# Kernel optimization log

Hardware: AMD Instinct MI355X
Metric: run time of the kernel (lower is better)

## Reference

```python
import jax, jax.numpy as jnp
import numpy as np

B = 16384  # batch
D = 1024   # input_size (== hidden_size, required by the original code)
H = 1024   # hidden_size


def setup_inputs() -> dict:
    key = jax.random.key(0)
    ks = jax.random.split(key, 20)
    s = 0.02
    inp = {
        "x": jax.random.normal(ks[0], (B, D), dtype=jnp.float32),
        "h": jax.random.normal(ks[1], (B, H), dtype=jnp.float32),
        "c_prev": jax.random.normal(ks[2], (B, H), dtype=jnp.float32),
    }
    names = ["i_x", "f_x", "c_x", "o_x", "i_h", "f_h", "c_h", "o_h"]
    for n, name in enumerate(names):
        in_dim = D if name.endswith("_x") else H
        inp["W" + name] = jax.random.normal(ks[3 + 2 * n], (H, in_dim), dtype=jnp.float32) * s
        inp["b" + name] = jax.random.normal(ks[4 + 2 * n], (H,), dtype=jnp.float32) * s
    return inp


def reference(x, h, c_prev,
              Wi_x, bi_x, Wf_x, bf_x, Wc_x, bc_x, Wo_x, bo_x,
              Wi_h, bi_h, Wf_h, bf_h, Wc_h, bc_h, Wo_h, bo_h):
    # NOTE: the original module applies NO sigmoid to the gates; i, f, o are raw affine sums.
    i = x @ Wi_x.T + bi_x + h @ Wi_h.T + bi_h
    f = x @ Wf_x.T + bf_x + h @ Wf_h.T + bf_h
    g = jnp.tanh(x @ Wc_x.T + bc_x + h @ Wc_h.T + bc_h)
    o = x @ Wo_x.T + bo_x + h @ Wo_h.T + bo_h
    c_next = g * i + c_prev * f
    h_next = o * jnp.tanh(c_next)
    return (h_next, c_next)
```

## Files before the change

kernel.cpp:

```cpp
#include <hip/hip_runtime.h>
#include <hip/hip_bf16.h>


#define MROWS 16384
#define NCOLS 1024
#define KTOT  2048

typedef __attribute__((ext_vector_type(8))) short bf16x8;
typedef __attribute__((ext_vector_type(4))) float f32x4;
typedef unsigned int u32;
typedef unsigned short u16;

__device__ __forceinline__ u16 f2bf(float f) {
  union { float f; u32 u; } v; v.f = f;
  u32 r = v.u + 0x7fffu + ((v.u >> 16) & 1u);
  return (u16)(r >> 16);
}

__device__ __forceinline__ bf16x8 pack8(float4 lo, float4 hi) {
  bf16x8 v;
  v[0] = (short)f2bf(lo.x); v[1] = (short)f2bf(lo.y);
  v[2] = (short)f2bf(lo.z); v[3] = (short)f2bf(lo.w);
  v[4] = (short)f2bf(hi.x); v[5] = (short)f2bf(hi.y);
  v[6] = (short)f2bf(hi.z); v[7] = (short)f2bf(hi.w);
  return v;
}

__device__ __forceinline__ float tanh_fast(float x) {
  float e = __expf(2.0f * x);
  return 1.0f - 2.0f / (e + 1.0f);
}

typedef __attribute__((address_space(1))) const u32 gas_u32;
typedef __attribute__((address_space(3))) u32 las_u32;

__device__ __forceinline__ void gl_lds16(const void* g, void* l) {
  __builtin_amdgcn_global_load_lds((gas_u32*)g, (las_u32*)l, 16, 0, 0);
}

__global__ void __launch_bounds__(256) convA(const float* __restrict__ x,
                                             const float* __restrict__ h,
                                             u16* __restrict__ A) {
  u32 t = blockIdx.x * 256u + threadIdx.x;
  #pragma unroll
  for (int i = 0; i < 4; ++i) {
    u32 chunk = t + (u32)i * 1048576u;
    u32 row = chunk >> 8;
    u32 cpos = (chunk & 255u) * 8u;
    const float* src = (cpos < 1024u) ? (x + (size_t)row * 1024 + cpos)
                                      : (h + (size_t)row * 1024 + (cpos - 1024u));
    float4 lo = *(const float4*)src;
    float4 hi = *(const float4*)(src + 4);
    *(bf16x8*)(A + (size_t)chunk * 8) = pack8(lo, hi);
  }
}

__global__ void __launch_bounds__(256) convW(const float* __restrict__ wix, const float* __restrict__ wfx,
                                             const float* __restrict__ wcx, const float* __restrict__ wox,
                                             const float* __restrict__ wih, const float* __restrict__ wfh,
                                             const float* __restrict__ wch, const float* __restrict__ woh,
                                             u16* __restrict__ W) {
  u32 t = blockIdx.x * 256u + threadIdx.x;
  const float* WX[4] = {wix, wfx, wcx, wox};
  const float* WH[4] = {wih, wfh, wch, woh};
  #pragma unroll
  for (int g = 0; g < 4; ++g) {
    u32 c3 = t;
    u32 n = c3 >> 8;
    u32 cpos = (c3 & 255u) * 8u;
    const float* src = (cpos < 1024u) ? (WX[g] + (size_t)n * 1024 + cpos)
                                      : (WH[g] + (size_t)n * 1024 + (cpos - 1024u));
    float4 lo = *(const float4*)src;
    float4 hi = *(const float4*)(src + 4);
    *(bf16x8*)(W + (size_t)g * 2097152 + (size_t)c3 * 8) = pack8(lo, hi);
  }
}

#define SBAR() __builtin_amdgcn_sched_barrier(0)

__global__ void __launch_bounds__(512) lstm_gemm8(
    const u16* __restrict__ Abf, const u16* __restrict__ Wbf,
    const float* __restrict__ bix, const float* __restrict__ bfx,
    const float* __restrict__ bcx, const float* __restrict__ box_,
    const float* __restrict__ bih, const float* __restrict__ bfh,
    const float* __restrict__ bch, const float* __restrict__ boh,
    const float* __restrict__ cprev, float* __restrict__ out) {
  __shared__ alignas(16) u16 sA[2 * 16384];
  __shared__ alignas(16) u16 sB[2 * 16384];

  const u32 tid = threadIdx.x;
  const u32 lane = tid & 63u, wid = tid >> 6;
  const u32 wr = wid >> 2, wc = wid & 3u;
  const u32 l15 = lane & 15u, l4 = lane >> 4;

  const u32 bid = blockIdx.x;
  const u32 sid = (bid & 7u) * 128u + (bid >> 3);
  const u32 bm = sid >> 4, bn = sid & 15u;

  const u16* gA[2][2];
  const u16* gB[2][2];
  #pragma unroll
  for (int h = 0; h < 2; ++h)
    #pragma unroll
    for (int j = 0; j < 2; ++j) {
      u32 chunk = (wid * 2u + (u32)j) * 64u + lane;
      u32 row = chunk >> 3, c = chunk & 7u;
      u32 col16 = c ^ (row & 7u);
      gA[h][j] = Abf + (size_t)(bm * 256u + (u32)h * 128u + row) * KTOT + col16 * 8u;
      u32 fr = (u32)h * 128u + row;
      u32 fi = fr >> 4;
      u32 Wrow = (fi & 3u) * 1024u + bn * 64u + (fi >> 2) * 16u + (fr & 15u);
      gB[h][j] = Wbf + (size_t)Wrow * KTOT + col16 * 8u;
    }

#define STAGE_A(ktile, dbuf) do { \
    gl_lds16(gA[0][0] + (ktile) * 64, sA + (dbuf) * 16384u + (wid * 2u + 0u) * 512u); \
    gl_lds16(gA[0][1] + (ktile) * 64, sA + (dbuf) * 16384u + (wid * 2u + 1u) * 512u); \
    gl_lds16(gA[1][0] + (ktile) * 64, sA + (dbuf) * 16384u + 8192u + (wid * 2u + 0u) * 512u); \
    gl_lds16(gA[1][1] + (ktile) * 64, sA + (dbuf) * 16384u + 8192u + (wid * 2u + 1u) * 512u); } while (0)
#define STAGE_B_H(ktile, dbuf, hh) do { \
    gl_lds16(gB[hh][0] + (ktile) * 64, sB + (dbuf) * 16384u + (hh) * 8192u + (wid * 2u + 0u) * 512u); \
    gl_lds16(gB[hh][1] + (ktile) * 64, sB + (dbuf) * 16384u + (hh) * 8192u + (wid * 2u + 1u) * 512u); } while (0)

  const char* cA = (const char*)sA;
  const char* cB = (const char*)sB;
  const u32 swzk[2] = { ((0u * 4u + l4) ^ (l15 & 7u)) << 4, ((1u * 4u + l4) ^ (l15 & 7u)) << 4 };

  f32x4 acc[8][4];
  #pragma unroll
  for (int mf = 0; mf < 8; ++mf)
    #pragma unroll
    for (int gf = 0; gf < 4; ++gf)
      acc[mf][gf] = (f32x4){0.f, 0.f, 0.f, 0.f};

  STAGE_A(0, 0);
  STAGE_B_H(0, 0, 0); STAGE_B_H(0, 0, 1);
  STAGE_A(1, 1);
  SBAR();
  asm volatile("s_waitcnt vmcnt(4)" ::: "memory");
  __builtin_amdgcn_s_barrier();
  SBAR();

  #pragma unroll 2
  for (int kt = 0; kt < 32; ++kt) {
    const u32 d = (u32)kt & 1u, dn = d ^ 1u;
    const u32 dA = d * 32768u, dB = d * 32768u;
    bf16x8 a03[4][2], a47[4][2], b01[2][2], b23[2][2];

    #pragma unroll
    for (int mf = 0; mf < 4; ++mf) {
      u32 rb = dA + (wr * 128u + (u32)mf * 16u + l15) * 128u;
      a03[mf][0] = *(const bf16x8*)(cA + rb + swzk[0]);
      a03[mf][1] = *(const bf16x8*)(cA + rb + swzk[1]);
    }
    #pragma unroll
    for (int gf = 0; gf < 2; ++gf) {
      u32 rb = dB + (wc * 64u + (u32)gf * 16u + l15) * 128u;
      b01[gf][0] = *(const bf16x8*)(cB + rb + swzk[0]);
      b01[gf][1] = *(const bf16x8*)(cB + rb + swzk[1]);
    }
    if (kt < 31) STAGE_B_H(kt + 1, dn, 0);
    SBAR();
    __builtin_amdgcn_s_barrier();
    asm volatile("s_waitcnt lgkmcnt(0)" ::: "memory");
    SBAR();
    __builtin_amdgcn_s_setprio(1);
    #pragma unroll
    for (int ks = 0; ks < 2; ++ks)
      #pragma unroll
      for (int gf = 0; gf < 2; ++gf)
        #pragma unroll
        for (int mf = 0; mf < 4; ++mf)
          acc[mf][gf] = __builtin_amdgcn_mfma_f32_16x16x32_bf16(a03[mf][ks], b01[gf][ks], acc[mf][gf], 0, 0, 0);
    __builtin_amdgcn_s_setprio(0);
    SBAR();
    __builtin_amdgcn_s_barrier();
    SBAR();

    #pragma unroll
    for (int gf = 0; gf < 2; ++gf) {
      u32 rb = dB + (wc * 64u + (2u + (u32)gf) * 16u + l15) * 128u;
      b23[gf][0] = *(const bf16x8*)(cB + rb + swzk[0]);
      b23[gf][1] = *(const bf16x8*)(cB + rb + swzk[1]);
    }
    if (kt < 31) STAGE_B_H(kt + 1, dn, 1);
    SBAR();
    __builtin_amdgcn_s_barrier();
    asm volatile("s_waitcnt lgkmcnt(0)" ::: "memory");
    SBAR();
    __builtin_amdgcn_s_setprio(1);
    #pragma unroll
    for (int ks = 0; ks < 2; ++ks)
      #pragma unroll
      for (int gf = 0; gf < 2; ++gf)
        #pragma unroll
        for (int mf = 0; mf < 4; ++mf)
          acc[mf][2 + gf] = __builtin_amdgcn_mfma_f32_16x16x32_bf16(a03[mf][ks], b23[gf][ks], acc[mf][2 + gf], 0, 0, 0);
    __builtin_amdgcn_s_setprio(0);
    SBAR();
    __builtin_amdgcn_s_barrier();
    SBAR();

    #pragma unroll
    for (int mf = 0; mf < 4; ++mf) {
      u32 rb = dA + (wr * 128u + (4u + (u32)mf) * 16u + l15) * 128u;
      a47[mf][0] = *(const bf16x8*)(cA + rb + swzk[0]);
      a47[mf][1] = *(const bf16x8*)(cA + rb + swzk[1]);
    }
    SBAR();
    __builtin_amdgcn_s_barrier();
    asm volatile("s_waitcnt lgkmcnt(0)" ::: "memory");
    SBAR();
    __builtin_amdgcn_s_setprio(1);
    #pragma unroll
    for (int ks = 0; ks < 2; ++ks)
      #pragma unroll
      for (int gf = 0; gf < 2; ++gf)
        #pragma unroll
        for (int mf = 0; mf < 4; ++mf)
          acc[4 + mf][gf] = __builtin_amdgcn_mfma_f32_16x16x32_bf16(a47[mf][ks], b01[gf][ks], acc[4 + mf][gf], 0, 0, 0);
    __builtin_amdgcn_s_setprio(0);
    SBAR();
    __builtin_amdgcn_s_barrier();
    SBAR();

    if (kt < 30) {
      STAGE_A(kt + 2, d);
      SBAR();
      asm volatile("s_waitcnt vmcnt(4)" ::: "memory");
    } else if (kt == 30) {
      SBAR();
      asm volatile("s_waitcnt vmcnt(0)" ::: "memory");
    }
    SBAR();
    __builtin_amdgcn_s_barrier();
    SBAR();
    __builtin_amdgcn_s_setprio(1);
    #pragma unroll
    for (int ks = 0; ks < 2; ++ks)
      #pragma unroll
      for (int gf = 0; gf < 2; ++gf)
        #pragma unroll
        for (int mf = 0; mf < 4; ++mf)
          acc[4 + mf][2 + gf] = __builtin_amdgcn_mfma_f32_16x16x32_bf16(a47[mf][ks], b23[gf][ks], acc[4 + mf][2 + gf], 0, 0, 0);
    __builtin_amdgcn_s_setprio(0);
    SBAR();
    __builtin_amdgcn_s_barrier();
    SBAR();
  }

  const u32 col = bn * 64u + wc * 16u + l15;
  const float bi = bix[col] + bih[col];
  const float bff = bfx[col] + bfh[col];
  const float bc = bcx[col] + bch[col];
  const float bo = box_[col] + boh[col];
  #pragma unroll
  for (int mf = 0; mf < 8; ++mf) {
    u32 row0 = bm * 256u + wr * 128u + (u32)mf * 16u + l4 * 4u;
    #pragma unroll
    for (int r = 0; r < 4; ++r) {
      size_t idx = (size_t)(row0 + (u32)r) * 1024 + col;
      float iv = acc[mf][0][r] + bi;
      float fv = acc[mf][1][r] + bff;
      float gv = tanh_fast(acc[mf][2][r] + bc);
      float ov = acc[mf][3][r] + bo;
      float cp = cprev[idx];
      float cn = gv * iv + cp * fv;
      out[idx] = ov * tanh_fast(cn);
      out[(size_t)16777216 + idx] = cn;
    }
  }
#undef STAGE_A
#undef STAGE_B_H
}

__global__ void __launch_bounds__(256, 2) lstm_gemm_fb(
    const float* __restrict__ x, const float* __restrict__ h,
    const float* __restrict__ wix, const float* __restrict__ wfx,
    const float* __restrict__ wcx, const float* __restrict__ wox,
    const float* __restrict__ wih, const float* __restrict__ wfh,
    const float* __restrict__ wch, const float* __restrict__ woh,
    const float* __restrict__ bix, const float* __restrict__ bfx,
    const float* __restrict__ bcx, const float* __restrict__ box_,
    const float* __restrict__ bih, const float* __restrict__ bfh,
    const float* __restrict__ bch, const float* __restrict__ boh,
    const float* __restrict__ cprev, float* __restrict__ out) {
  __shared__ alignas(16) u16 sA[128 * 64];
  __shared__ alignas(16) u16 sB[4 * 64 * 64];
  const u32 tid = threadIdx.x;
  const u32 lane = tid & 63u;
  const u32 wid = tid >> 6;
  const u32 wr = wid >> 1, wc = wid & 1u;
  const u32 bidx = blockIdx.x;
  const u32 bm = bidx >> 4, bn = bidx & 15u;
  f32x4 acc[4][4][2];
  #pragma unroll
  for (int g = 0; g < 4; ++g)
    #pragma unroll
    for (int m = 0; m < 4; ++m)
      #pragma unroll
      for (int n = 0; n < 2; ++n)
        acc[g][m][n] = (f32x4){0.f, 0.f, 0.f, 0.f};
  const u32 l15 = lane & 15u, l4 = lane >> 4;
  for (int kt = 0; kt < KTOT / 64; ++kt) {
    const u32 k0 = (u32)kt * 64u;
    if (kt) __syncthreads();
    #pragma unroll
    for (int c = 0; c < 4; ++c) {
      u32 chunk = tid + (u32)c * 256u;
      u32 row = chunk >> 3;
      u32 cp = (chunk & 7u) * 8u;
      u32 gk = k0 + cp;
      const float* src = (gk < 1024u) ? (x + (size_t)(bm * 128u + row) * 1024 + gk)
                                      : (h + (size_t)(bm * 128u + row) * 1024 + (gk - 1024u));
      float4 lo = *(const float4*)src;
      float4 hi = *(const float4*)(src + 4);
      u32 dst = row * 128u + ((cp * 2u) ^ ((row & 7u) << 4));
      *(bf16x8*)((char*)sA + dst) = pack8(lo, hi);
    }
    #pragma unroll
    for (int g = 0; g < 4; ++g) {
      const float* Wxg = (g == 0) ? wix : (g == 1) ? wfx : (g == 2) ? wcx : wox;
      const float* Whg = (g == 0) ? wih : (g == 1) ? wfh : (g == 2) ? wch : woh;
      #pragma unroll
      for (int cc = 0; cc < 2; ++cc) {
        u32 c3 = tid + (u32)cc * 256u;
        u32 row = c3 >> 3;
        u32 cp = (c3 & 7u) * 8u;
        u32 gk = k0 + cp;
        const float* src = (gk < 1024u) ? (Wxg + (size_t)(bn * 64u + row) * 1024 + gk)
                                        : (Whg + (size_t)(bn * 64u + row) * 1024 + (gk - 1024u));
        float4 lo = *(const float4*)src;
        float4 hi = *(const float4*)(src + 4);
        u32 dst = (u32)g * 8192u + row * 128u + ((cp * 2u) ^ ((row & 7u) << 4));
        *(bf16x8*)((char*)sB + dst) = pack8(lo, hi);
      }
    }
    __syncthreads();
    #pragma unroll
    for (int s = 0; s < 2; ++s) {
      bf16x8 af[4];
      #pragma unroll
      for (int m = 0; m < 4; ++m) {
        u32 mrow = wr * 64u + (u32)m * 16u + l15;
        u32 off = mrow * 128u + (((u32)s * 64u + l4 * 16u) ^ ((mrow & 7u) << 4));
        af[m] = *(const bf16x8*)((const char*)sA + off);
      }
      #pragma unroll
      for (int g = 0; g < 4; ++g) {
        #pragma unroll
        for (int nf = 0; nf < 2; ++nf) {
          u32 nrow = wc * 32u + (u32)nf * 16u + l15;
          u32 off = (u32)g * 8192u + nrow * 128u +
                    (((u32)s * 64u + l4 * 16u) ^ ((nrow & 7u) << 4));
          bf16x8 bfr = *(const bf16x8*)((const char*)sB + off);
          #pragma unroll
          for (int m = 0; m < 4; ++m)
            acc[g][m][nf] = __builtin_amdgcn_mfma_f32_16x16x32_bf16(af[m], bfr, acc[g][m][nf], 0, 0, 0);
        }
      }
    }
  }
  #pragma unroll
  for (int nf = 0; nf < 2; ++nf) {
    u32 col = bn * 64u + wc * 32u + (u32)nf * 16u + l15;
    float bi = bix[col] + bih[col];
    float bff = bfx[col] + bfh[col];
    float bc = bcx[col] + bch[col];
    float bo = box_[col] + boh[col];
    #pragma unroll
    for (int m = 0; m < 4; ++m) {
      u32 row0 = bm * 128u + wr * 64u + (u32)m * 16u + l4 * 4u;
      #pragma unroll
      for (int r = 0; r < 4; ++r) {
        size_t idx = (size_t)(row0 + (u32)r) * 1024 + col;
        float iv = acc[0][m][nf][r] + bi;
        float fv = acc[1][m][nf][r] + bff;
        float gv = tanh_fast(acc[2][m][nf][r] + bc);
        float ov = acc[3][m][nf][r] + bo;
        float cp = cprev[idx];
        float cn = gv * iv + cp * fv;
        out[idx] = ov * tanh_fast(cn);
        out[(size_t)16777216 + idx] = cn;
      }
    }
  }
}

extern "C" void kernel_launch(void* const* d_in, const int* in_sizes, int n_in,
                              void* d_out, int out_size, void* d_ws, size_t ws_size,
                              hipStream_t stream) {
  const float* x = (const float*)d_in[0];
  const float* h = (const float*)d_in[1];
  const float* cprev = (const float*)d_in[2];
  const float* wix = (const float*)d_in[3];  const float* bix = (const float*)d_in[4];
  const float* wfx = (const float*)d_in[5];  const float* bfx = (const float*)d_in[6];
  const float* wcx = (const float*)d_in[7];  const float* bcx = (const float*)d_in[8];
  const float* wox = (const float*)d_in[9];  const float* box_ = (const float*)d_in[10];
  const float* wih = (const float*)d_in[11]; const float* bih = (const float*)d_in[12];
  const float* wfh = (const float*)d_in[13]; const float* bfh = (const float*)d_in[14];
  const float* wch = (const float*)d_in[15]; const float* bch = (const float*)d_in[16];
  const float* woh = (const float*)d_in[17]; const float* boh = (const float*)d_in[18];
  float* out = (float*)d_out;

  const size_t needA = (size_t)MROWS * KTOT * 2;
  const size_t needW = (size_t)4 * NCOLS * KTOT * 2;

  if (ws_size >= needA + needW) {
    u16* Abf = (u16*)d_ws;
    u16* Wbf = (u16*)((char*)d_ws + needA);
    convA<<<dim3(4096), dim3(256), 0, stream>>>(x, h, Abf);
    convW<<<dim3(1024), dim3(256), 0, stream>>>(wix, wfx, wcx, wox, wih, wfh, wch, woh, Wbf);
    lstm_gemm8<<<dim3(1024), dim3(512), 0, stream>>>(
        Abf, Wbf, bix, bfx, bcx, box_, bih, bfh, bch, boh, cprev, out);
  } else {
    lstm_gemm_fb<<<dim3(2048), dim3(256), 0, stream>>>(
        x, h, wix, wfx, wcx, wox, wih, wfh, wch, woh,
        bix, bfx, bcx, box_, bih, bfh, bch, boh, cprev, out);
  }
}
```

Measured before the change: 342.3 us.

## Prefetch B tiles two stages ahead and drop redundant scheduling barriers

```diff
diff --git a/kernel.cpp b/kernel.cpp
--- a/kernel.cpp
+++ b/kernel.cpp
@@ -118,9 +118,11 @@
     gl_lds16(gA[0][1] + (ktile) * 64, sA + (dbuf) * 16384u + (wid * 2u + 1u) * 512u); \
     gl_lds16(gA[1][0] + (ktile) * 64, sA + (dbuf) * 16384u + 8192u + (wid * 2u + 0u) * 512u); \
     gl_lds16(gA[1][1] + (ktile) * 64, sA + (dbuf) * 16384u + 8192u + (wid * 2u + 1u) * 512u); } while (0)
-#define STAGE_B_H(ktile, dbuf, hh) do { \
-    gl_lds16(gB[hh][0] + (ktile) * 64, sB + (dbuf) * 16384u + (hh) * 8192u + (wid * 2u + 0u) * 512u); \
-    gl_lds16(gB[hh][1] + (ktile) * 64, sB + (dbuf) * 16384u + (hh) * 8192u + (wid * 2u + 1u) * 512u); } while (0)
+#define STAGE_B(ktile, dbuf) do { \
+    gl_lds16(gB[0][0] + (ktile) * 64, sB + (dbuf) * 16384u + (wid * 2u + 0u) * 512u); \
+    gl_lds16(gB[0][1] + (ktile) * 64, sB + (dbuf) * 16384u + (wid * 2u + 1u) * 512u); \
+    gl_lds16(gB[1][0] + (ktile) * 64, sB + (dbuf) * 16384u + 8192u + (wid * 2u + 0u) * 512u); \
+    gl_lds16(gB[1][1] + (ktile) * 64, sB + (dbuf) * 16384u + 8192u + (wid * 2u + 1u) * 512u); } while (0)
 
   const char* cA = (const char*)sA;
   const char* cB = (const char*)sB;
@@ -133,34 +135,29 @@
     for (int gf = 0; gf < 4; ++gf)
       acc[mf][gf] = (f32x4){0.f, 0.f, 0.f, 0.f};
 
-  STAGE_A(0, 0);
-  STAGE_B_H(0, 0, 0); STAGE_B_H(0, 0, 1);
-  STAGE_A(1, 1);
-  SBAR();
-  asm volatile("s_waitcnt vmcnt(4)" ::: "memory");
+  STAGE_B(0, 0); STAGE_A(0, 0);
+  STAGE_B(1, 1); STAGE_A(1, 1);
+  asm volatile("s_waitcnt vmcnt(8)" ::: "memory");
   __builtin_amdgcn_s_barrier();
-  SBAR();
 
   #pragma unroll 2
   for (int kt = 0; kt < 32; ++kt) {
-    const u32 d = (u32)kt & 1u, dn = d ^ 1u;
-    const u32 dA = d * 32768u, dB = d * 32768u;
+    const u32 d = (u32)kt & 1u;
+    const u32 dO = d * 32768u;
     bf16x8 a03[4][2], a47[4][2], b01[2][2], b23[2][2];
 
     #pragma unroll
     for (int mf = 0; mf < 4; ++mf) {
-      u32 rb = dA + (wr * 128u + (u32)mf * 16u + l15) * 128u;
+      u32 rb = dO + (wr * 128u + (u32)mf * 16u + l15) * 128u;
       a03[mf][0] = *(const bf16x8*)(cA + rb + swzk[0]);
       a03[mf][1] = *(const bf16x8*)(cA + rb + swzk[1]);
     }
     #pragma unroll
     for (int gf = 0; gf < 2; ++gf) {
-      u32 rb = dB + (wc * 64u + (u32)gf * 16u + l15) * 128u;
+      u32 rb = dO + (wc * 64u + (u32)gf * 16u + l15) * 128u;
       b01[gf][0] = *(const bf16x8*)(cB + rb + swzk[0]);
       b01[gf][1] = *(const bf16x8*)(cB + rb + swzk[1]);
     }
-    if (kt < 31) STAGE_B_H(kt + 1, dn, 0);
-    SBAR();
     __builtin_amdgcn_s_barrier();
     asm volatile("s_waitcnt lgkmcnt(0)" ::: "memory");
     SBAR();
@@ -173,18 +170,14 @@
         for (int mf = 0; mf < 4; ++mf)
           acc[mf][gf] = __builtin_amdgcn_mfma_f32_16x16x32_bf16(a03[mf][ks], b01[gf][ks], acc[mf][gf], 0, 0, 0);
     __builtin_amdgcn_s_setprio(0);
-    SBAR();
-    __builtin_amdgcn_s_barrier();
-    SBAR();
+    __builtin_amdgcn_s_barrier();
 
     #pragma unroll
     for (int gf = 0; gf < 2; ++gf) {
-      u32 rb = dB + (wc * 64u + (2u + (u32)gf) * 16u + l15) * 128u;
+      u32 rb = dO + (wc * 64u + (2u + (u32)gf) * 16u + l15) * 128u;
       b23[gf][0] = *(const bf16x8*)(cB + rb + swzk[0]);
       b23[gf][1] = *(const bf16x8*)(cB + rb + swzk[1]);
     }
-    if (kt < 31) STAGE_B_H(kt + 1, dn, 1);
-    SBAR();
     __builtin_amdgcn_s_barrier();
     asm volatile("s_waitcnt lgkmcnt(0)" ::: "memory");
     SBAR();
@@ -197,17 +190,15 @@
         for (int mf = 0; mf < 4; ++mf)
           acc[mf][2 + gf] = __builtin_amdgcn_mfma_f32_16x16x32_bf16(a03[mf][ks], b23[gf][ks], acc[mf][2 + gf], 0, 0, 0);
     __builtin_amdgcn_s_setprio(0);
-    SBAR();
-    __builtin_amdgcn_s_barrier();
-    SBAR();
-
+    __builtin_amdgcn_s_barrier();
+
+    if (kt < 30) STAGE_B(kt + 2, d);
     #pragma unroll
     for (int mf = 0; mf < 4; ++mf) {
-      u32 rb = dA + (wr * 128u + (4u + (u32)mf) * 16u + l15) * 128u;
+      u32 rb = dO + (wr * 128u + (4u + (u32)mf) * 16u + l15) * 128u;
       a47[mf][0] = *(const bf16x8*)(cA + rb + swzk[0]);
       a47[mf][1] = *(const bf16x8*)(cA + rb + swzk[1]);
     }
-    SBAR();
     __builtin_amdgcn_s_barrier();
     asm volatile("s_waitcnt lgkmcnt(0)" ::: "memory");
     SBAR();
@@ -220,21 +211,15 @@
         for (int mf = 0; mf < 4; ++mf)
           acc[4 + mf][gf] = __builtin_amdgcn_mfma_f32_16x16x32_bf16(a47[mf][ks], b01[gf][ks], acc[4 + mf][gf], 0, 0, 0);
     __builtin_amdgcn_s_setprio(0);
-    SBAR();
-    __builtin_amdgcn_s_barrier();
-    SBAR();
+    __builtin_amdgcn_s_barrier();
 
     if (kt < 30) {
       STAGE_A(kt + 2, d);
-      SBAR();
-      asm volatile("s_waitcnt vmcnt(4)" ::: "memory");
+      asm volatile("s_waitcnt vmcnt(8)" ::: "memory");
     } else if (kt == 30) {
-      SBAR();
       asm volatile("s_waitcnt vmcnt(0)" ::: "memory");
     }
-    SBAR();
-    __builtin_amdgcn_s_barrier();
-    SBAR();
+    __builtin_amdgcn_s_barrier();
     __builtin_amdgcn_s_setprio(1);
     #pragma unroll
     for (int ks = 0; ks < 2; ++ks)
@@ -244,9 +229,7 @@
         for (int mf = 0; mf < 4; ++mf)
           acc[4 + mf][2 + gf] = __builtin_amdgcn_mfma_f32_16x16x32_bf16(a47[mf][ks], b23[gf][ks], acc[4 + mf][2 + gf], 0, 0, 0);
     __builtin_amdgcn_s_setprio(0);
-    SBAR();
-    __builtin_amdgcn_s_barrier();
-    SBAR();
+    __builtin_amdgcn_s_barrier();
   }
 
   const u32 col = bn * 64u + wc * 16u + l15;
@@ -271,7 +254,7 @@
     }
   }
 #undef STAGE_A
-#undef STAGE_B_H
+#undef STAGE_B
 }
 
 __global__ void __launch_bounds__(256, 2) lstm_gemm_fb(
```

Measured after the change: 337.0 us. About the same (-1.6%).
